# Performance work log

Measured on AMD Instinct MI355X. Metric: run time of the kernel, lower is better.

Reference implementation:

```python
import jax, jax.numpy as jnp
import numpy as np

B, S, IN_DIM, HID = 8, 2048, 1024, 1024


def setup_inputs() -> dict:
    key = jax.random.key(0)
    k1, k2, k3, k4, k5 = jax.random.split(key, 5)
    vec = jax.random.normal(k1, (B, S, IN_DIM), dtype=jnp.float32)
    # nn.Linear-style init scale
    wq_w = jax.random.normal(k2, (HID, IN_DIM), dtype=jnp.float32) / np.sqrt(IN_DIM)
    wq_b = jax.random.normal(k3, (HID,), dtype=jnp.float32) * 0.02
    lin_w = jax.random.normal(k4, (1, HID), dtype=jnp.float32) / np.sqrt(HID)
    lin_b = jax.random.normal(k5, (1,), dtype=jnp.float32) * 0.02
    return {"vec": vec, "wq_w": wq_w, "wq_b": wq_b, "lin_w": lin_w, "lin_b": lin_b}


def reference(vec, wq_w, wq_b, lin_w, lin_b):
    # NOTE: the original forward applies self.wq to BOTH q and k (wk/nq/nk unused).
    q = jnp.einsum('bsi,hi->bsh', vec, wq_w) + wq_b          # [B,S,H]
    ret = jnp.einsum('bsx,bsy->bxy', q, q)                    # [B,H,H] bilinear
    ret = jax.nn.relu(ret)
    out = jnp.einsum('bxy,y->bx', ret, lin_w[0]) + lin_b[0]   # Linear(H,1) -> [B,H]
    return out
```

## Files before the change

kernel.cpp:

```cpp
#include <hip/hip_runtime.h>


typedef short     bf16x8 __attribute__((ext_vector_type(8)));
typedef unsigned short u16x8 __attribute__((ext_vector_type(8)));
typedef float     f32x4 __attribute__((ext_vector_type(4)));
typedef long long i64;

#define FENCE asm volatile("" ::: "memory")
#define BARR  do { FENCE; __builtin_amdgcn_s_barrier(); FENCE; } while (0)
#define VMCNT(N) asm volatile("s_waitcnt vmcnt(" #N ")" ::: "memory")

__device__ inline unsigned short f2bf(float f) {
  unsigned int u = __float_as_uint(f);
  u += 0x7fffu + ((u >> 16) & 1u);
  return (unsigned short)(u >> 16);
}

__device__ inline u16x8 pack8(float4 a, float4 b) {
  u16x8 r;
  r[0] = f2bf(a.x); r[1] = f2bf(a.y); r[2] = f2bf(a.z); r[3] = f2bf(a.w);
  r[4] = f2bf(b.x); r[5] = f2bf(b.y); r[6] = f2bf(b.z); r[7] = f2bf(b.w);
  return r;
}

__device__ inline unsigned char f2fp8(float v) {
  int pk = __builtin_amdgcn_cvt_pk_fp8_f32(v, v, 0, false);
  return (unsigned char)(pk & 0xff);
}

__device__ inline void async16(void* lds, const void* g) {
  __builtin_amdgcn_global_load_lds(
      (const __attribute__((address_space(1))) void*)g,
      (__attribute__((address_space(3))) void*)lds,
      16, 0, 0);
}

__global__ __launch_bounds__(256) void prep(
    const float* __restrict__ vec, unsigned short* __restrict__ vecbf,
    const float* __restrict__ wq,  unsigned short* __restrict__ wqbf,
    const float* __restrict__ lin_b, float* __restrict__ out)
{
  if (blockIdx.x < 8192) {
    const int c   = ((blockIdx.x & 7) << 10) + (blockIdx.x >> 3);
    const int gid = c * 256 + threadIdx.x;
    const float4* s = (const float4*)(vec + (size_t)gid * 8);
    float4 a = s[0], b = s[1];
    *(u16x8*)(vecbf + (size_t)gid * 8) = pack8(a, b);
    const int oid = blockIdx.x * 256 + threadIdx.x;
    if (oid < 8192) out[oid] = lin_b[0];
  } else {
    const int i = (blockIdx.x - 8192) * 256 + threadIdx.x;
    const float4* s = (const float4*)(wq + (size_t)i * 8);
    float4 a = s[0], b = s[1];
    *(u16x8*)(wqbf + (size_t)i * 8) = pack8(a, b);
  }
}

__global__ void init_out(float* __restrict__ out, const float* __restrict__ lin_b) {
  int i = blockIdx.x * 256 + threadIdx.x;
  if (i < 8192) out[i] = lin_b[0];
}

__global__ __launch_bounds__(512, 2) void gemm_1p(
    const unsigned short* __restrict__ A, const unsigned short* __restrict__ Bm,
    const float* __restrict__ bias, unsigned char* __restrict__ qT8)
{
  __shared__ unsigned short As[2][256 * 64];
  __shared__ unsigned short Bs[2][256 * 64];

  const int bid = blockIdx.y * 64 + blockIdx.x;
  const int xcd = bid & 7;
  const int idx = bid >> 3;
  const int m0 = (idx & 3) * 256;
  const int n0 = (xcd * 8 + (idx >> 2)) * 256;

  const int t    = threadIdx.x;
  const int lane = t & 63;
  const int wave = t >> 6;
  const int wm2  = (wave >> 2) * 64;
  const int wn2  = (wave & 3) * 32;
  const int quad = lane >> 4;
  const int lrow = lane & 15;

  const int srow = t >> 3;
  const int gch  = (t & 7) ^ (srow & 7);
  const unsigned short* gA = A  + (size_t)(m0 + srow) * 1024 + gch * 8;
  const unsigned short* gB = Bm + (size_t)(n0 + srow) * 1024 + gch * 8;

#define STAGE_A(SLOT, H, KT) do { \
  _Pragma("unroll") for (int p = 0; p < 2; ++p) \
    async16(&As[SLOT][((H)*128 + p*64)*64 + t*8], \
            gA + (size_t)((H)*128 + p*64)*1024 + (KT)*64); \
} while (0)

#define STAGE_B(SLOT, H, KT) do { \
  _Pragma("unroll") for (int p = 0; p < 2; ++p) \
    async16(&Bs[SLOT][((H)*128 + p*64)*64 + t*8], \
            gB + (size_t)((H)*128 + p*64)*1024 + (KT)*64); \
} while (0)

#define LDA_HALF(S, MH) do { \
  _Pragma("unroll") for (int f = 0; f < 4; ++f) \
  _Pragma("unroll") for (int kk = 0; kk < 2; ++kk) \
    a_[f][kk] = *(const bf16x8*)&As[S][((MH)*128 + wm2 + f*16 + lrow)*64 + \
                                       (((kk*4 + quad) ^ (lrow & 7)) * 8)]; \
} while (0)

#define LDB_HALF(S, NH, BREG) do { \
  _Pragma("unroll") for (int g = 0; g < 2; ++g) \
  _Pragma("unroll") for (int kk = 0; kk < 2; ++kk) \
    BREG[g][kk] = *(const bf16x8*)&Bs[S][((NH)*128 + wn2 + g*16 + lrow)*64 + \
                                         (((kk*4 + quad) ^ (lrow & 7)) * 8)]; \
} while (0)

#define MFMAQ(MH, NH, BREG) do { \
  __builtin_amdgcn_s_setprio(1); \
  _Pragma("unroll") for (int kk = 0; kk < 2; ++kk) \
  _Pragma("unroll") for (int f = 0; f < 4; ++f) \
  _Pragma("unroll") for (int g = 0; g < 2; ++g) \
    acc[MH][f][NH][g] = __builtin_amdgcn_mfma_f32_16x16x32_bf16( \
        a_[f][kk], BREG[g][kk], acc[MH][f][NH][g], 0, 0, 0); \
  __builtin_amdgcn_s_setprio(0); \
} while (0)

  f32x4 acc[2][4][2][2];
#pragma unroll
  for (int i = 0; i < 2; ++i)
#pragma unroll
    for (int f = 0; f < 4; ++f)
#pragma unroll
      for (int j = 0; j < 2; ++j)
#pragma unroll
        for (int g = 0; g < 2; ++g) acc[i][f][j][g] = (f32x4){0.f, 0.f, 0.f, 0.f};

  bf16x8 a_[4][2], b0_[2][2], b1_[2][2];

  STAGE_A(0, 0, 0);
  STAGE_B(0, 0, 0);
  STAGE_A(0, 1, 0);
  STAGE_B(0, 1, 0);

#pragma unroll 1
  for (int kt = 0; kt < 15; ++kt) {
    const int s  = kt & 1;
    const int so = s ^ 1;

    STAGE_A(so, 0, kt + 1);
    STAGE_B(so, 0, kt + 1);
    STAGE_A(so, 1, kt + 1);
    STAGE_B(so, 1, kt + 1);
    VMCNT(8);
    BARR;

    LDA_HALF(s, 0);
    LDB_HALF(s, 0, b0_);
    MFMAQ(0, 0, b0_);
    LDB_HALF(s, 1, b1_);
    MFMAQ(0, 1, b1_);
    LDA_HALF(s, 1);
    MFMAQ(1, 0, b0_);
    MFMAQ(1, 1, b1_);
    BARR;
  }

  VMCNT(0);
  BARR;
  LDA_HALF(1, 0);
  LDB_HALF(1, 0, b0_);
  MFMAQ(0, 0, b0_);
  LDB_HALF(1, 1, b1_);
  MFMAQ(0, 1, b1_);
  LDA_HALF(1, 1);
  MFMAQ(1, 0, b0_);
  MFMAQ(1, 1, b1_);

#pragma unroll
  for (int mh = 0; mh < 2; ++mh)
#pragma unroll
    for (int f = 0; f < 4; ++f)
#pragma unroll
      for (int r = 0; r < 4; ++r) {
        const int m = m0 + mh * 128 + wm2 + f * 16 + quad * 4 + r;
        const float bv = bias[m];
        unsigned char* row = qT8 + (size_t)m * 16384 + n0;
#pragma unroll
        for (int nh = 0; nh < 2; ++nh)
#pragma unroll
          for (int g = 0; g < 2; ++g)
            row[nh * 128 + wn2 + g * 16 + lrow] = f2fp8(acc[mh][f][nh][g][r] + bv);
      }

#undef STAGE_A
#undef STAGE_B
#undef LDA_HALF
#undef LDB_HALF
#undef MFMAQ
}

__global__ __launch_bounds__(256) void gemm_q_fused(
    const float* __restrict__ Wq, const float* __restrict__ V,
    const float* __restrict__ bias, unsigned char* __restrict__ qT8)
{
  __shared__ unsigned short As[128 * 32];
  __shared__ unsigned short Bs[128 * 32];

  const int m0 = blockIdx.y * 128;
  const int n0 = blockIdx.x * 128;
  const int t    = threadIdx.x;
  const int lane = t & 63;
  const int wave = t >> 6;
  const int wm = (wave >> 1) * 64;
  const int wn = (wave & 1) * 64;
  const int quad = lane >> 4;
  const int lrow = lane & 15;

  const int sr = t >> 1;
  const int sc = (t & 1) << 4;
  const float* gA = Wq + (size_t)(m0 + sr) * 1024 + sc;
  const float* gB = V  + (size_t)(n0 + sr) * 1024 + sc;

  f32x4 acc[4][4];
#pragma unroll
  for (int i = 0; i < 4; ++i)
#pragma unroll
    for (int j = 0; j < 4; ++j) acc[i][j] = (f32x4){0.f, 0.f, 0.f, 0.f};

  for (int k0 = 0; k0 < 1024; k0 += 32) {
    const float4* a4 = (const float4*)(gA + k0);
    const float4* b4 = (const float4*)(gB + k0);
    float4 av0 = a4[0], av1 = a4[1], av2 = a4[2], av3 = a4[3];
    float4 bv0 = b4[0], bv1 = b4[1], bv2 = b4[2], bv3 = b4[3];
    *(u16x8*)&As[sr * 32 + sc]     = pack8(av0, av1);
    *(u16x8*)&As[sr * 32 + sc + 8] = pack8(av2, av3);
    *(u16x8*)&Bs[sr * 32 + sc]     = pack8(bv0, bv1);
    *(u16x8*)&Bs[sr * 32 + sc + 8] = pack8(bv2, bv3);
    __syncthreads();

    bf16x8 af[4], bfr[4];
#pragma unroll
    for (int i = 0; i < 4; ++i)
      af[i] = *(const bf16x8*)&As[(wm + i * 16 + lrow) * 32 + quad * 8];
#pragma unroll
    for (int j = 0; j < 4; ++j)
      bfr[j] = *(const bf16x8*)&Bs[(wn + j * 16 + lrow) * 32 + quad * 8];
#pragma unroll
    for (int i = 0; i < 4; ++i)
#pragma unroll
      for (int j = 0; j < 4; ++j)
        acc[i][j] = __builtin_amdgcn_mfma_f32_16x16x32_bf16(af[i], bfr[j], acc[i][j], 0, 0, 0);
    __syncthreads();
  }

#pragma unroll
  for (int i = 0; i < 4; ++i) {
    const int mb = m0 + wm + i * 16 + quad * 4;
#pragma unroll
    for (int r = 0; r < 4; ++r) {
      const float bv = bias[mb + r];
#pragma unroll
      for (int j = 0; j < 4; ++j) {
        const int n = n0 + wn + j * 16 + lrow;
        qT8[(size_t)(mb + r) * 16384 + n] = f2fp8(acc[i][j][r] + bv);
      }
    }
  }
}

__global__ __launch_bounds__(256) void syrk_half8(
    const unsigned char* __restrict__ qT8, const float* __restrict__ W,
    float* __restrict__ out)
{
  __shared__ unsigned char As[2][128 * 128];
  __shared__ unsigned char Bs[2][64 * 128];

  const int bb   = blockIdx.x & 7;
  const int id2  = blockIdx.x >> 3;
  const int pair = id2 >> 1;
  const int yh   = id2 & 1;
  int tx = 0;
  while ((tx + 1) * (tx + 2) / 2 <= pair) ++tx;
  const int ty = pair - tx * (tx + 1) / 2;
  const int x0 = tx * 128;
  const int y0 = ty * 128 + yh * 64;
  const bool diag = (tx == ty);

  const int t    = threadIdx.x;
  const int lane = t & 63;
  const int wave = t >> 6;
  const int wm = (wave >> 1) * 64;
  const int wn = (wave & 1) * 32;
  const int quad = lane >> 4;
  const int lrow = lane & 15;

  const int srow = t >> 3;
  const int g16  = (t & 7) ^ (srow & 7);
  const size_t cb = (size_t)bb * 2048 + g16 * 16;
  const unsigned char* gA = qT8 + (size_t)(x0 + srow) * 16384 + cb;
  const unsigned char* gB = qT8 + (size_t)(y0 + srow) * 16384 + cb;

#define SSTAGE(SLOT, KT) do { \
  _Pragma("unroll") for (int p = 0; p < 4; ++p) \
    async16(&As[SLOT][p * 4096 + t * 16], gA + (size_t)p * 32 * 16384 + (KT) * 128); \
  _Pragma("unroll") for (int p = 0; p < 2; ++p) \
    async16(&Bs[SLOT][p * 4096 + t * 16], gB + (size_t)p * 32 * 16384 + (KT) * 128); \
} while (0)

#define SYRK_COMPUTE(S) do { \
  _Pragma("unroll") for (int kk = 0; kk < 4; ++kk) { \
    const int c = kk * 4 + quad; \
    const int off = (((c >> 1) ^ (lrow & 7)) << 4) + (c & 1) * 8; \
    i64 af[4], bfr[2]; \
    _Pragma("unroll") for (int i = 0; i < 4; ++i) \
      af[i] = *(const i64*)&As[S][(wm + i * 16 + lrow) * 128 + off]; \
    _Pragma("unroll") for (int j = 0; j < 2; ++j) \
      bfr[j] = *(const i64*)&Bs[S][(wn + j * 16 + lrow) * 128 + off]; \
    _Pragma("unroll") for (int i = 0; i < 4; ++i) \
      _Pragma("unroll") for (int j = 0; j < 2; ++j) \
        acc[i][j] = __builtin_amdgcn_mfma_f32_16x16x32_fp8_fp8(af[i], bfr[j], acc[i][j], 0, 0, 0); \
  } \
} while (0)

  f32x4 acc[4][2];
#pragma unroll
  for (int i = 0; i < 4; ++i)
#pragma unroll
    for (int j = 0; j < 2; ++j) acc[i][j] = (f32x4){0.f, 0.f, 0.f, 0.f};

  SSTAGE(0, 0);

#pragma unroll 1
  for (int kt = 0; kt < 15; ++kt) {
    const int s = kt & 1;
    SSTAGE(s ^ 1, kt + 1);
    VMCNT(6);
    BARR;
    SYRK_COMPUTE(s);
    BARR;
  }

  VMCNT(0);
  BARR;
  SYRK_COMPUTE(1);

#undef SSTAGE
#undef SYRK_COMPUTE

  float* ob = out + bb * 1024;

  float wv[2];
#pragma unroll
  for (int j = 0; j < 2; ++j) wv[j] = W[y0 + wn + j * 16 + lrow];

#pragma unroll
  for (int i = 0; i < 4; ++i) {
#pragma unroll
    for (int r = 0; r < 4; ++r) {
      float p = 0.f;
#pragma unroll
      for (int j = 0; j < 2; ++j) {
        float v = acc[i][j][r];
        v = v > 0.f ? v : 0.f;
        p += v * wv[j];
      }
#pragma unroll
      for (int off = 1; off < 16; off <<= 1) p += __shfl_xor(p, off, 64);
      if (lrow == 0)
        atomicAdd(&ob[x0 + wm + i * 16 + quad * 4 + r], p);
    }
  }

  if (!diag) {
    float wx[4][4];
#pragma unroll
    for (int i = 0; i < 4; ++i)
#pragma unroll
      for (int r = 0; r < 4; ++r)
        wx[i][r] = W[x0 + wm + i * 16 + quad * 4 + r];

#pragma unroll
    for (int j = 0; j < 2; ++j) {
      float pc = 0.f;
#pragma unroll
      for (int i = 0; i < 4; ++i)
#pragma unroll
        for (int r = 0; r < 4; ++r) {
          float v = acc[i][j][r];
          v = v > 0.f ? v : 0.f;
          pc += v * wx[i][r];
        }
      pc += __shfl_xor(pc, 16, 64);
      pc += __shfl_xor(pc, 32, 64);
      if (quad == 0)
        atomicAdd(&ob[y0 + wn + j * 16 + lrow], pc);
    }
  }
}

extern "C" void kernel_launch(void* const* d_in, const int* in_sizes, int n_in,
                              void* d_out, int out_size, void* d_ws, size_t ws_size,
                              hipStream_t stream) {
  const float* vec   = (const float*)d_in[0];
  const float* wq_w  = (const float*)d_in[1];
  const float* wq_b  = (const float*)d_in[2];
  const float* lin_w = (const float*)d_in[3];
  const float* lin_b = (const float*)d_in[4];
  float* out = (float*)d_out;

  unsigned char* qT8 = (unsigned char*)d_ws;
  const size_t need = (size_t)(16 + 32 + 2) * 1024 * 1024;

  if (ws_size >= need) {
    unsigned short* vecbf = (unsigned short*)((char*)d_ws + (size_t)16 * 1024 * 1024);
    unsigned short* wqbf  = vecbf + (size_t)16 * 1024 * 1024;
    prep<<<dim3(8192 + 512), dim3(256), 0, stream>>>(vec, vecbf, wq_w, wqbf, lin_b, out);
    gemm_1p<<<dim3(64, 4), dim3(512), 0, stream>>>(wqbf, vecbf, wq_b, qT8);
  } else {
    init_out<<<dim3(32), dim3(256), 0, stream>>>(out, lin_b);
    gemm_q_fused<<<dim3(128, 8), dim3(256), 0, stream>>>(wq_w, vec, wq_b, qT8);
  }
  syrk_half8<<<dim3(576), dim3(256), 0, stream>>>(qT8, lin_w, out);
}
```

Measured before the change: 163.8 us.

## Replace LDS-staged SYRK with direct global-to-register fp8 MFMA loads

The SYRK kernel stops staging q tiles through double-buffered shared memory with async copies and barriers. Each wave now loads its fp8 fragments straight from global memory into registers, and the block tile is split along x instead of y (64x128). This removes the LDS traffic and barrier synchronisation. In exchange there is no data reuse across waves in a block, so global/L2 traffic rises and the 8-byte strided loads may be poorly coalesced.

```diff
diff --git a/kernel.cpp b/kernel.cpp
--- a/kernel.cpp
+++ b/kernel.cpp
@@ -266,132 +266,109 @@
   }
 }
 
-__global__ __launch_bounds__(256) void syrk_half8(
+__global__ __launch_bounds__(256) void syrk_direct(
     const unsigned char* __restrict__ qT8, const float* __restrict__ W,
     float* __restrict__ out)
 {
-  __shared__ unsigned char As[2][128 * 128];
-  __shared__ unsigned char Bs[2][64 * 128];
-
   const int bb   = blockIdx.x & 7;
   const int id2  = blockIdx.x >> 3;
   const int pair = id2 >> 1;
-  const int yh   = id2 & 1;
+  const int xh   = id2 & 1;
   int tx = 0;
   while ((tx + 1) * (tx + 2) / 2 <= pair) ++tx;
   const int ty = pair - tx * (tx + 1) / 2;
-  const int x0 = tx * 128;
-  const int y0 = ty * 128 + yh * 64;
+  const int x0 = tx * 128 + xh * 64;
+  const int y0 = ty * 128;
   const bool diag = (tx == ty);
 
   const int t    = threadIdx.x;
   const int lane = t & 63;
   const int wave = t >> 6;
-  const int wm = (wave >> 1) * 64;
-  const int wn = (wave & 1) * 32;
+  const int wx   = (wave >> 1) * 32;
+  const int wy   = (wave & 1) * 64;
   const int quad = lane >> 4;
   const int lrow = lane & 15;
 
-  const int srow = t >> 3;
-  const int g16  = (t & 7) ^ (srow & 7);
-  const size_t cb = (size_t)bb * 2048 + g16 * 16;
-  const unsigned char* gA = qT8 + (size_t)(x0 + srow) * 16384 + cb;
-  const unsigned char* gB = qT8 + (size_t)(y0 + srow) * 16384 + cb;
-
-#define SSTAGE(SLOT, KT) do { \
-  _Pragma("unroll") for (int p = 0; p < 4; ++p) \
-    async16(&As[SLOT][p * 4096 + t * 16], gA + (size_t)p * 32 * 16384 + (KT) * 128); \
-  _Pragma("unroll") for (int p = 0; p < 2; ++p) \
-    async16(&Bs[SLOT][p * 4096 + t * 16], gB + (size_t)p * 32 * 16384 + (KT) * 128); \
-} while (0)
-
-#define SYRK_COMPUTE(S) do { \
-  _Pragma("unroll") for (int kk = 0; kk < 4; ++kk) { \
-    const int c = kk * 4 + quad; \
-    const int off = (((c >> 1) ^ (lrow & 7)) << 4) + (c & 1) * 8; \
-    i64 af[4], bfr[2]; \
-    _Pragma("unroll") for (int i = 0; i < 4; ++i) \
-      af[i] = *(const i64*)&As[S][(wm + i * 16 + lrow) * 128 + off]; \
-    _Pragma("unroll") for (int j = 0; j < 2; ++j) \
-      bfr[j] = *(const i64*)&Bs[S][(wn + j * 16 + lrow) * 128 + off]; \
-    _Pragma("unroll") for (int i = 0; i < 4; ++i) \
-      _Pragma("unroll") for (int j = 0; j < 2; ++j) \
-        acc[i][j] = __builtin_amdgcn_mfma_f32_16x16x32_fp8_fp8(af[i], bfr[j], acc[i][j], 0, 0, 0); \
-  } \
-} while (0)
-
-  f32x4 acc[4][2];
-#pragma unroll
-  for (int i = 0; i < 4; ++i)
-#pragma unroll
-    for (int j = 0; j < 2; ++j) acc[i][j] = (f32x4){0.f, 0.f, 0.f, 0.f};
-
-  SSTAGE(0, 0);
-
-#pragma unroll 1
-  for (int kt = 0; kt < 15; ++kt) {
-    const int s = kt & 1;
-    SSTAGE(s ^ 1, kt + 1);
-    VMCNT(6);
-    BARR;
-    SYRK_COMPUTE(s);
-    BARR;
-  }
-
-  VMCNT(0);
-  BARR;
-  SYRK_COMPUTE(1);
-
-#undef SSTAGE
-#undef SYRK_COMPUTE
+  const unsigned char* base = qT8 + (size_t)bb * 2048 + quad * 8;
+  const unsigned char* gA = base + (size_t)(x0 + wx + lrow) * 16384;
+  const unsigned char* gB = base + (size_t)(y0 + wy + lrow) * 16384;
+
+  f32x4 acc[2][4];
+#pragma unroll
+  for (int m = 0; m < 2; ++m)
+#pragma unroll
+    for (int j = 0; j < 4; ++j) acc[m][j] = (f32x4){0.f, 0.f, 0.f, 0.f};
+
+#pragma unroll 2
+  for (int k0 = 0; k0 < 2048; k0 += 128) {
+    i64 a[2][4], b[4][4];
+#pragma unroll
+    for (int m = 0; m < 2; ++m)
+#pragma unroll
+      for (int kk = 0; kk < 4; ++kk)
+        a[m][kk] = *(const i64*)(gA + (size_t)m * 16 * 16384 + k0 + kk * 32);
+#pragma unroll
+    for (int j = 0; j < 4; ++j)
+#pragma unroll
+      for (int kk = 0; kk < 4; ++kk)
+        b[j][kk] = *(const i64*)(gB + (size_t)j * 16 * 16384 + k0 + kk * 32);
+#pragma unroll
+    for (int kk = 0; kk < 4; ++kk)
+#pragma unroll
+      for (int m = 0; m < 2; ++m)
+#pragma unroll
+        for (int j = 0; j < 4; ++j)
+          acc[m][j] = __builtin_amdgcn_mfma_f32_16x16x32_fp8_fp8(
+              a[m][kk], b[j][kk], acc[m][j], 0, 0, 0);
+  }
 
   float* ob = out + bb * 1024;
 
-  float wv[2];
-#pragma unroll
-  for (int j = 0; j < 2; ++j) wv[j] = W[y0 + wn + j * 16 + lrow];
-
-#pragma unroll
-  for (int i = 0; i < 4; ++i) {
+  float wv[4];
+#pragma unroll
+  for (int j = 0; j < 4; ++j) wv[j] = W[y0 + wy + j * 16 + lrow];
+
+#pragma unroll
+  for (int m = 0; m < 2; ++m) {
 #pragma unroll
     for (int r = 0; r < 4; ++r) {
       float p = 0.f;
 #pragma unroll
-      for (int j = 0; j < 2; ++j) {
-        float v = acc[i][j][r];
+      for (int j = 0; j < 4; ++j) {
+        float v = acc[m][j][r];
         v = v > 0.f ? v : 0.f;
         p += v * wv[j];
       }
 #pragma unroll
       for (int off = 1; off < 16; off <<= 1) p += __shfl_xor(p, off, 64);
       if (lrow == 0)
-        atomicAdd(&ob[x0 + wm + i * 16 + quad * 4 + r], p);
+        atomicAdd(&ob[x0 + wx + m * 16 + quad * 4 + r], p);
     }
   }
 
   if (!diag) {
-    float wx[4][4];
-#pragma unroll
-    for (int i = 0; i < 4; ++i)
+    float wxr[2][4];
+#pragma unroll
+    for (int m = 0; m < 2; ++m)
 #pragma unroll
       for (int r = 0; r < 4; ++r)
-        wx[i][r] = W[x0 + wm + i * 16 + quad * 4 + r];
-
-#pragma unroll
-    for (int j = 0; j < 2; ++j) {
+        wxr[m][r] = W[x0 + wx + m * 16 + quad * 4 + r];
+
+#pragma unroll
+    for (int j = 0; j < 4; ++j) {
       float pc = 0.f;
 #pragma unroll
-      for (int i = 0; i < 4; ++i)
+      for (int m = 0; m < 2; ++m)
 #pragma unroll
         for (int r = 0; r < 4; ++r) {
-          float v = acc[i][j][r];
+          float v = acc[m][j][r];
           v = v > 0.f ? v : 0.f;
-          pc += v * wx[i][r];
+          pc += v * wxr[m][r];
         }
       pc += __shfl_xor(pc, 16, 64);
       pc += __shfl_xor(pc, 32, 64);
       if (quad == 0)
-        atomicAdd(&ob[y0 + wn + j * 16 + lrow], pc);
+        atomicAdd(&ob[y0 + wy + j * 16 + lrow], pc);
     }
   }
 }
@@ -418,5 +395,5 @@
     init_out<<<dim3(32), dim3(256), 0, stream>>>(out, lin_b);
     gemm_q_fused<<<dim3(128, 8), dim3(256), 0, stream>>>(wq_w, vec, wq_b, qT8);
   }
-  syrk_half8<<<dim3(576), dim3(256), 0, stream>>>(qT8, lin_w, out);
-}
+  syrk_direct<<<dim3(576), dim3(256), 0, stream>>>(qT8, lin_w, out);
+}
```

Result: slower. 268.6 us (+64.0%).
